# Kernel tuning notes

Measured on AMD Instinct MI355X. Metric: run time of the kernel, lower is better.

The kernel has to match this reference:

```python
import jax, jax.numpy as jnp
import numpy as np

N, H, HEADS = 4096, 256, 3
ALPHA = 0.2
NEG_INF = -9e15


def _sign_adj(key, n, density):
    # sparse signed adjacency with +1 on the diagonal (values in {-1,0,1})
    k1, k2 = jax.random.split(key)
    mask = jax.random.uniform(k1, (n, n)) < density
    sign = jnp.where(jax.random.uniform(k2, (n, n)) < 0.5, -1.0, 1.0)
    adj = jnp.where(mask, sign, 0.0).astype(jnp.float32)
    idx = jnp.arange(n)
    return adj.at[idx, idx].set(1.0)


def setup_inputs() -> dict:
    key = jax.random.key(0)
    ks = jax.random.split(key, 16)
    std = 0.01
    gain = 1.414
    return {
        "h": jax.random.normal(ks[0], (N, H), jnp.float32),
        "node_adj": _sign_adj(ks[1], N, 0.005),
        "edge_adj": _sign_adj(ks[2], N, 0.005),
        "gat_W": jax.random.normal(ks[3], (HEADS, H, H), jnp.float32) * (gain / np.sqrt(H, dtype=np.float32)),
        "gat_a": jax.random.normal(ks[4], (HEADS, 2 * H, 1), jnp.float32) * 0.1,
        "edge_Wih": jax.random.normal(ks[5], (3 * H, H), jnp.float32) * std,
        "edge_Whh": jax.random.normal(ks[6], (3 * H, H), jnp.float32) * std,
        "edge_bih": jnp.zeros((3 * H,), jnp.float32),
        "edge_bhh": jnp.zeros((3 * H,), jnp.float32),
        "node_Wih": jax.random.normal(ks[7], (3 * H, H), jnp.float32) * std,
        "node_Whh": jax.random.normal(ks[8], (3 * H, H), jnp.float32) * std,
        "node_bih": jnp.zeros((3 * H,), jnp.float32),
        "node_bhh": jnp.zeros((3 * H,), jnp.float32),
    }


def _gru_cell(x, hstate, Wih, Whh, bih, bhh):
    # torch.nn.GRUCell math, gate order [r, z, n]
    gi = x @ Wih.T + bih
    gh = hstate @ Whh.T + bhh
    ir, iz, inn = jnp.split(gi, 3, axis=1)
    hr, hz, hn = jnp.split(gh, 3, axis=1)
    r = jax.nn.sigmoid(ir + hr)
    z = jax.nn.sigmoid(iz + hz)
    n = jnp.tanh(inn + r * hn)
    return (1.0 - z) * n + z * hstate


def _gat_head(h, node_adj, edge_adj, W, a):
    hW = h @ W  # [N,H]
    hp = (node_adj > 0).astype(hW.dtype) @ hW
    hm = (node_adj < 0).astype(hW.dtype) @ hW
    e_plus = jax.nn.leaky_relu(jnp.concatenate([hp, hm], axis=1) @ a, ALPHA)[:, 0]   # [N]
    e_minus = jax.nn.leaky_relu(jnp.concatenate([hm, hp], axis=1) @ a, ALPHA)[:, 0]  # [N]
    # attention[i, j] depends only on column j (original builds this via repeat)
    att = jnp.where(edge_adj > 0, e_plus[None, :], NEG_INF)
    att = jnp.where(edge_adj < 0, e_minus[None, :], att)
    att = jax.nn.softmax(att, axis=1)
    return (att * edge_adj) @ hW  # concat=False -> no elu


def reference(h, node_adj, edge_adj, gat_W, gat_a,
              edge_Wih, edge_Whh, edge_bih, edge_bhh,
              node_Wih, node_Whh, node_bih, node_bhh):
    dn = jnp.diag(node_adj)  # [N]
    de = jnp.diag(edge_adj)  # [N]
    idx = jnp.arange(node_adj.shape[0])
    node_adj_norm = node_adj.at[idx, idx].add(-dn)  # zero diagonal
    edge_adj_norm = edge_adj.at[idx, idx].add(-de)

    # msg_type == 'diff'
    node_support = node_adj_norm @ h
    edge_output = _gru_cell(node_support, h, edge_Wih, edge_Whh, edge_bih, edge_bhh)

    edge_support = _gat_head(h, node_adj_norm, edge_adj_norm, gat_W[0], gat_a[0])
    for i in range(1, HEADS):
        edge_support = edge_support + _gat_head(h, node_adj_norm, edge_adj_norm, gat_W[i], gat_a[i])
    edge_support = edge_support / HEADS

    node_output = _gru_cell(edge_support, h, node_Wih, node_Whh, node_bih, node_bhh)

    # sp.mm(I_edge, edge_output) + sp.mm(I_node, node_output)
    return de[:, None] * edge_output + dn[:, None] * node_output
```

## Files before the change

### kernel.cpp

```cpp
#include <hip/hip_runtime.h>
#include <hip/hip_bf16.h>
#include <math.h>

#define NN 4096
#define HH 256
#define G3 768
#define NHEADS 3
#define MAXE 128
#define ALPHA 0.2f

typedef __bf16 bf16;
typedef __attribute__((ext_vector_type(2))) __bf16 bf16x2;
typedef __attribute__((ext_vector_type(4))) __bf16 bf16x4;
typedef __attribute__((ext_vector_type(8))) __bf16 bf16x8;
typedef __attribute__((ext_vector_type(4))) float f32x4;

__device__ __forceinline__ void async_copy16(void* lds, const void* g) {
    __builtin_amdgcn_global_load_lds((const __attribute__((address_space(1))) void*)g,
                                     (__attribute__((address_space(3))) void*)lds, 16, 0, 0);
}

__device__ inline float lrelu(float x) { return x > 0.f ? x : ALPHA * x; }
__device__ inline float sigm(float x) { return 1.f / (1.f + __expf(-x)); }

__global__ __launch_bounds__(256) void prep_k(
    const float* __restrict__ h,
    const float* __restrict__ eWih, const float* __restrict__ eWhh,
    const float* __restrict__ nWih, const float* __restrict__ nWhh,
    const float* __restrict__ gat_W, const float* __restrict__ gat_a,
    bf16* __restrict__ hb,
    bf16* __restrict__ Weib, bf16* __restrict__ Wehb,
    bf16* __restrict__ Wnib, bf16* __restrict__ Wnhb,
    bf16* __restrict__ Wtb, float* __restrict__ c0, float* __restrict__ c1) {
    __shared__ float tile[32][33];
    __shared__ float a_s[512];
    int b = blockIdx.x, t = threadIdx.x;
    if (b < 1024) {
        int idx = b * 256 + t;
        float4 v = *(const float4*)(h + (size_t)idx * 4);
        bf16x4 o = {(bf16)v.x, (bf16)v.y, (bf16)v.z, (bf16)v.w};
        *(bf16x4*)(hb + (size_t)idx * 4) = o;
    } else if (b < 1792) {
        int w = (b - 1024) / 192;
        int idx = ((b - 1024) % 192) * 256 + t;
        const float* in = w == 0 ? eWih : (w == 1 ? eWhh : (w == 2 ? nWih : nWhh));
        bf16* outp = w == 0 ? Weib : (w == 1 ? Wehb : (w == 2 ? Wnib : Wnhb));
        float4 v = *(const float4*)(in + (size_t)idx * 4);
        bf16x4 o = {(bf16)v.x, (bf16)v.y, (bf16)v.z, (bf16)v.w};
        *(bf16x4*)(outp + (size_t)idx * 4) = o;
    } else if (b < 1984) {
        int b2 = b - 1792;
        int hd = b2 >> 6, tl = b2 & 63;
        int k0 = (tl >> 3) * 32, n0 = (tl & 7) * 32;
        int tx = t % 32, ty = t / 32;
        const float* Wh = gat_W + (size_t)hd * HH * HH;
        for (int r = ty; r < 32; r += 8) tile[r][tx] = Wh[(size_t)(k0 + r) * HH + n0 + tx];
        __syncthreads();
        bf16* Wth = Wtb + (size_t)hd * HH * HH;
        for (int r = ty; r < 32; r += 8) Wth[(size_t)(n0 + r) * HH + k0 + tx] = (bf16)tile[tx][r];
    } else {
        int hd = b - 1984;
        a_s[t] = gat_a[(size_t)hd * 512 + t];
        a_s[t + 256] = gat_a[(size_t)hd * 512 + 256 + t];
        __syncthreads();
        const float* Wr = gat_W + (size_t)hd * HH * HH + (size_t)t * HH;
        f32x4 s0v = {}, s1v = {};
#pragma unroll 8
        for (int c4 = 0; c4 < 64; c4++) {
            f32x4 w = *(const f32x4*)(Wr + c4 * 4);
            f32x4 a0 = *(const f32x4*)(a_s + c4 * 4);
            f32x4 a1 = *(const f32x4*)(a_s + 256 + c4 * 4);
            s0v += w * a0;
            s1v += w * a1;
        }
        c0[hd * HH + t] = s0v[0] + s0v[1] + s0v[2] + s0v[3];
        c1[hd * HH + t] = s1v[0] + s1v[1] + s1v[2] + s1v[3];
    }
}

__global__ __launch_bounds__(256) void scan_k(
    const float* __restrict__ node_adj, const float* __restrict__ edge_adj,
    const bf16* __restrict__ hb,
    const float* __restrict__ c0, const float* __restrict__ c1,
    bf16* __restrict__ nsupb, float* __restrict__ dn, float* __restrict__ de,
    float* __restrict__ ep, float* __restrict__ em,
    int* __restrict__ csr_cols, int* __restrict__ csr_nnz) {
    __shared__ float buf[2][NN];
    __shared__ int cnt[2];
    __shared__ int colsbuf[2][MAXE];
    __shared__ float part[6][4];
    int t = threadIdx.x, lane = t & 63, wid = t >> 6;
    int r0 = blockIdx.x * 2;

    if (t == 0) { cnt[0] = 0; cnt[1] = 0; }

    {
        const float* src = node_adj + (size_t)r0 * NN + t * 4;
        float* dst = &buf[0][t * 4];
#pragma unroll
        for (int q = 0; q < 4; q++) async_copy16(dst + q * 1024, src + q * 1024);
    }
    __syncthreads();

#pragma unroll
    for (int tk = 0; tk < 4; tk++) {
        int par = tk & 1;
        int i = r0 + (tk >> 1);
        bool node_t = (par == 0);

        if (tk < 3) {
            int ntk = tk + 1;
            int nrow = r0 + (ntk >> 1);
            const float* src = ((ntk & 1) ? edge_adj : node_adj) + (size_t)nrow * NN + t * 4;
            float* dst = &buf[ntk & 1][t * 4];
#pragma unroll
            for (int q = 0; q < 4; q++) async_copy16(dst + q * 1024, src + q * 1024);
        }

        float wv[16];
#pragma unroll
        for (int q = 0; q < 16; q++) wv[q] = buf[par][q * 256 + t];

        int k = 0;
#pragma unroll
        for (int q = 0; q < 16; q++) {
            int j = q * 256 + t;
            if (wv[q] != 0.f) {
                if (j == i) (node_t ? dn : de)[i] = wv[q];
                else k++;
            }
        }
        int base = 0;
        if (k) base = atomicAdd(&cnt[par], k);
#pragma unroll
        for (int q = 0; q < 16; q++) {
            int j = q * 256 + t;
            if (wv[q] != 0.f && j != i) {
                if (base < MAXE) colsbuf[par][base] = (wv[q] > 0.f) ? (j + 1) : -(j + 1);
                base++;
            }
        }
        __syncthreads();
        int n = cnt[par];
        if (n > MAXE) n = MAXE;

        if (node_t) {
            float accp = 0.f, accm = 0.f;
#pragma unroll 8
            for (int kk = 0; kk < n; kk++) {
                int c = colsbuf[par][kk];
                int j = (c > 0 ? c : -c) - 1;
                float hv = (float)hb[(size_t)j * HH + t];
                if (c > 0) accp += hv; else accm += hv;
            }
            nsupb[(size_t)i * HH + t] = (bf16)(accp - accm);
            float u[6];
#pragma unroll
            for (int hd = 0; hd < NHEADS; hd++) {
                float a0 = c0[hd * HH + t], a1 = c1[hd * HH + t];
                u[hd * 2]     = accp * a0 + accm * a1;
                u[hd * 2 + 1] = accm * a0 + accp * a1;
            }
#pragma unroll
            for (int vv = 0; vv < 6; vv++)
#pragma unroll
                for (int off = 32; off; off >>= 1) u[vv] += __shfl_xor(u[vv], off);
            if (lane == 0)
#pragma unroll
                for (int vv = 0; vv < 6; vv++) part[vv][wid] = u[vv];
            __syncthreads();
            if (t < 6) {
                float s = part[t][0] + part[t][1] + part[t][2] + part[t][3];
                int hd = t >> 1;
                ((t & 1) == 0 ? ep : em)[(size_t)hd * NN + i] = lrelu(s);
            }
        } else {
            if (t == 0) csr_nnz[i] = n;
            if (t < n) csr_cols[(size_t)i * MAXE + t] = colsbuf[par][t];
        }
        __syncthreads();
        if (t == 0) cnt[par] = 0;
    }
}

__global__ __launch_bounds__(256) void gemm_bt(
    const bf16* __restrict__ A0, const bf16* __restrict__ A1, const bf16* __restrict__ A2,
    const bf16* __restrict__ B0, const bf16* __restrict__ B1, const bf16* __restrict__ B2,
    bf16* __restrict__ C0, bf16* __restrict__ C1, bf16* __restrict__ C2) {
    __shared__ bf16 a_s[128 * 32];
    __shared__ bf16 b_s[128 * 32];
    int z = blockIdx.z;
    const bf16* A = z == 0 ? A0 : (z == 1 ? A1 : A2);
    const bf16* Bt = z == 0 ? B0 : (z == 1 ? B1 : B2);
    bf16* C = z == 0 ? C0 : (z == 1 ? C1 : C2);

    int tid = threadIdx.x;
    int lane = tid & 63, wid = tid >> 6;
    int wr = (wid >> 1) * 64, wc = (wid & 1) * 64;
    int i0 = blockIdx.x * 128;
    int c0n = blockIdx.y * 128;

    f32x4 acc[4][4] = {};
    int kq = (lane >> 4) * 8;

    for (int k0 = 0; k0 < 256; k0 += 32) {
        __syncthreads();
#pragma unroll
        for (int it = 0; it < 2; it++) {
            int ch = it * 256 + tid;
            int r = ch >> 2, c16 = ch & 3;
            async_copy16(&a_s[ch * 8], A + (size_t)(i0 + r) * 256 + k0 + c16 * 8);
            async_copy16(&b_s[ch * 8], Bt + (size_t)(c0n + r) * 256 + k0 + c16 * 8);
        }
        __syncthreads();
        bf16x8 af[4], bf[4];
#pragma unroll
        for (int m = 0; m < 4; m++) af[m] = *(const bf16x8*)&a_s[(wr + m * 16 + (lane & 15)) * 32 + kq];
#pragma unroll
        for (int n = 0; n < 4; n++) bf[n] = *(const bf16x8*)&b_s[(wc + n * 16 + (lane & 15)) * 32 + kq];
#pragma unroll
        for (int m = 0; m < 4; m++)
#pragma unroll
            for (int n = 0; n < 4; n++)
                acc[m][n] = __builtin_amdgcn_mfma_f32_16x16x32_bf16(af[m], bf[n], acc[m][n], 0, 0, 0);
    }
#pragma unroll
    for (int m = 0; m < 4; m++) {
#pragma unroll
        for (int n = 0; n < 4; n++) {
            int row = i0 + wr + m * 16 + (lane >> 4) * 4;
            int col = c0n + wc + n * 16 + (lane & 15);
#pragma unroll
            for (int j = 0; j < 4; j++)
                C[(size_t)(row + j) * G3 + col] = (bf16)acc[m][n][j];
        }
    }
}

__global__ __launch_bounds__(256) void gat_out(
    const int* __restrict__ csr_cols, const int* __restrict__ csr_nnz,
    const float* __restrict__ ep, const float* __restrict__ em,
    const bf16* __restrict__ hWb2, bf16* __restrict__ esupb) {
    int i = blockIdx.x, t = threadIdx.x;
    __shared__ int cols_s[MAXE];
    __shared__ int js[MAXE];
    __shared__ float w_s[NHEADS][MAXE];
    __shared__ f32x4 sacc[NHEADS][64];
    int n = csr_nnz[i];
    if (t < n) {
        int c = csr_cols[(size_t)i * MAXE + t];
        cols_s[t] = c;
        js[t] = (c > 0 ? c : -c) - 1;
    }
    __syncthreads();
    int wid = t >> 6, lane = t & 63;
    if (wid < NHEADS) {
        int hd = wid;
        const float* eph = ep + (size_t)hd * NN;
        const float* emh = em + (size_t)hd * NN;
        float v0 = -1e30f, v1 = -1e30f;
        if (lane < n)      { int c = cols_s[lane];      v0 = c > 0 ? eph[js[lane]]      : emh[js[lane]]; }
        if (lane + 64 < n) { int c = cols_s[lane + 64]; v1 = c > 0 ? eph[js[lane + 64]] : emh[js[lane + 64]]; }
        float mx = fmaxf(v0, v1);
#pragma unroll
        for (int off = 32; off; off >>= 1) mx = fmaxf(mx, __shfl_xor(mx, off));
        float w0 = (lane < n) ? __expf(v0 - mx) : 0.f;
        float w1 = (lane + 64 < n) ? __expf(v1 - mx) : 0.f;
        float s = w0 + w1;
#pragma unroll
        for (int off = 32; off; off >>= 1) s += __shfl_xor(s, off);
        float inv = 1.f / s;
        if (lane < n)      w_s[hd][lane]      = (cols_s[lane] > 0 ? w0 : -w0) * inv;
        if (lane + 64 < n) w_s[hd][lane + 64] = (cols_s[lane + 64] > 0 ? w1 : -w1) * inv;
    }
    __syncthreads();
    if (t < 192) {
        int hd = t >> 6, g = t & 63;
        const bf16* base = hWb2 + (size_t)hd * HH + g * 4;
        f32x4 acc = {};
#pragma unroll 4
        for (int k = 0; k < n; k++) {
            float w = w_s[hd][k];
            bf16x4 hv = *(const bf16x4*)(base + (size_t)js[k] * G3);
            f32x4 f = {(float)hv[0], (float)hv[1], (float)hv[2], (float)hv[3]};
            acc += w * f;
        }
        sacc[hd][g] = acc;
    }
    __syncthreads();
    if (t < 64) {
        f32x4 s = (sacc[0][t] + sacc[1][t] + sacc[2][t]) * (1.f / 3.f);
        bf16x4 o = {(bf16)s[0], (bf16)s[1], (bf16)s[2], (bf16)s[3]};
        *(bf16x4*)(esupb + (size_t)i * HH + t * 4) = o;
    }
}

__global__ __launch_bounds__(256) void gru_both(
    const bf16* __restrict__ gie, const bf16* __restrict__ ghe,
    const bf16* __restrict__ gin, const bf16* __restrict__ ghn,
    const float* __restrict__ ebih, const float* __restrict__ ebhh,
    const float* __restrict__ nbih, const float* __restrict__ nbhh,
    const float* __restrict__ h, const float* __restrict__ dnv, const float* __restrict__ dev,
    float* __restrict__ out) {
    int sub = threadIdx.x >> 7, tc = threadIdx.x & 127;
    int i = blockIdx.x * 2 + sub;
    int c = tc * 2;
    size_t gb = (size_t)i * G3;
    float2 hv = *(const float2*)(h + (size_t)i * HH + c);
    float De = dev[i], Dn = dnv[i];

#define LD2(p, off) (*(const bf16x2*)((p) + gb + (off) + c))
#define BI2(p, off) (*(const float2*)((p) + (off) + c))
    bf16x2 eir = LD2(gie, 0), eiz = LD2(gie, 256), ein = LD2(gie, 512);
    bf16x2 ehr = LD2(ghe, 0), ehz = LD2(ghe, 256), ehn = LD2(ghe, 512);
    bf16x2 nir = LD2(gin, 0), niz = LD2(gin, 256), nin = LD2(gin, 512);
    bf16x2 nhr = LD2(ghn, 0), nhz = LD2(ghn, 256), nhn = LD2(ghn, 512);
    float2 ebr = BI2(ebih, 0), ebz = BI2(ebih, 256), ebn = BI2(ebih, 512);
    float2 eb2r = BI2(ebhh, 0), eb2z = BI2(ebhh, 256), eb2n = BI2(ebhh, 512);
    float2 nbr = BI2(nbih, 0), nbz = BI2(nbih, 256), nbn = BI2(nbih, 512);
    float2 nb2r = BI2(nbhh, 0), nb2z = BI2(nbhh, 256), nb2n = BI2(nbhh, 512);
#undef LD2
#undef BI2

    float res[2];
#pragma unroll
    for (int j = 0; j < 2; j++) {
        float hj = j == 0 ? hv.x : hv.y;
        float r = sigm(((float)eir[j] + (j ? ebr.y : ebr.x)) + ((float)ehr[j] + (j ? eb2r.y : eb2r.x)));
        float z = sigm(((float)eiz[j] + (j ? ebz.y : ebz.x)) + ((float)ehz[j] + (j ? eb2z.y : eb2z.x)));
        float nv = tanhf(((float)ein[j] + (j ? ebn.y : ebn.x)) + r * ((float)ehn[j] + (j ? eb2n.y : eb2n.x)));
        float eo = (1.f - z) * nv + z * hj;
        float r2 = sigm(((float)nir[j] + (j ? nbr.y : nbr.x)) + ((float)nhr[j] + (j ? nb2r.y : nb2r.x)));
        float z2 = sigm(((float)niz[j] + (j ? nbz.y : nbz.x)) + ((float)nhz[j] + (j ? nb2z.y : nb2z.x)));
        float nv2 = tanhf(((float)nin[j] + (j ? nbn.y : nbn.x)) + r2 * ((float)nhn[j] + (j ? nb2n.y : nb2n.x)));
        float no = (1.f - z2) * nv2 + z2 * hj;
        res[j] = De * eo + Dn * no;
    }
    *(float2*)(out + (size_t)i * HH + c) = make_float2(res[0], res[1]);
}

extern "C" void kernel_launch(void* const* d_in, const int* in_sizes, int n_in,
                              void* d_out, int out_size, void* d_ws, size_t ws_size,
                              hipStream_t stream) {
    const float* h        = (const float*)d_in[0];
    const float* node_adj = (const float*)d_in[1];
    const float* edge_adj = (const float*)d_in[2];
    const float* gat_W    = (const float*)d_in[3];
    const float* gat_a    = (const float*)d_in[4];
    const float* e_Wih    = (const float*)d_in[5];
    const float* e_Whh    = (const float*)d_in[6];
    const float* e_bih    = (const float*)d_in[7];
    const float* e_bhh    = (const float*)d_in[8];
    const float* n_Wih    = (const float*)d_in[9];
    const float* n_Whh    = (const float*)d_in[10];
    const float* n_bih    = (const float*)d_in[11];
    const float* n_bhh    = (const float*)d_in[12];
    float* out = (float*)d_out;

    char* ws = (char*)d_ws;
    size_t off = 0;
    auto alloc = [&](size_t bytes) { char* p = ws + off; off += (bytes + 255) & ~(size_t)255; return p; };

    float* ep    = (float*)alloc((size_t)NHEADS * NN * 4);
    float* em    = (float*)alloc((size_t)NHEADS * NN * 4);
    float* c0    = (float*)alloc((size_t)NHEADS * HH * 4);
    float* c1    = (float*)alloc((size_t)NHEADS * HH * 4);
    float* dn    = (float*)alloc(NN * 4);
    float* de    = (float*)alloc(NN * 4);
    bf16*  hb    = (bf16*)alloc((size_t)NN * HH * 2);
    bf16*  nsupb = (bf16*)alloc((size_t)NN * HH * 2);
    bf16*  esupb = (bf16*)alloc((size_t)NN * HH * 2);
    bf16*  hWb2  = (bf16*)alloc((size_t)NN * G3 * 2);
    bf16*  gie   = (bf16*)alloc((size_t)NN * G3 * 2);
    bf16*  ghe   = (bf16*)alloc((size_t)NN * G3 * 2);
    bf16*  gin   = (bf16*)alloc((size_t)NN * G3 * 2);
    bf16*  ghn   = (bf16*)alloc((size_t)NN * G3 * 2);
    bf16*  Weib  = (bf16*)alloc((size_t)G3 * HH * 2);
    bf16*  Wehb  = (bf16*)alloc((size_t)G3 * HH * 2);
    bf16*  Wnib  = (bf16*)alloc((size_t)G3 * HH * 2);
    bf16*  Wnhb  = (bf16*)alloc((size_t)G3 * HH * 2);
    bf16*  Wtb   = (bf16*)alloc((size_t)NHEADS * HH * HH * 2);
    int*   csr_cols = (int*)alloc((size_t)NN * MAXE * 4);
    int*   csr_nnz  = (int*)alloc(NN * 4);

    dim3 b256(256);

    prep_k<<<1987, b256, 0, stream>>>(h, e_Wih, e_Whh, n_Wih, n_Whh, gat_W, gat_a,
                                      hb, Weib, Wehb, Wnib, Wnhb, Wtb, c0, c1);

    scan_k<<<NN / 2, b256, 0, stream>>>(node_adj, edge_adj, hb, c0, c1,
                                        nsupb, dn, de, ep, em, csr_cols, csr_nnz);

    gemm_bt<<<dim3(NN / 128, G3 / 128, 3), b256, 0, stream>>>(
        hb, nsupb, hb, Wtb, Weib, Wehb, hWb2, gie, ghe);

    gat_out<<<NN, b256, 0, stream>>>(csr_cols, csr_nnz, ep, em, hWb2, esupb);

    gemm_bt<<<dim3(NN / 128, G3 / 128, 2), b256, 0, stream>>>(
        esupb, hb, hb, Wnib, Wnhb, Wnhb, gin, ghn, ghn);

    gru_both<<<NN / 2, b256, 0, stream>>>(gie, ghe, gin, ghn,
                                          e_bih, e_bhh, n_bih, n_bhh,
                                          h, dn, de, out);
}
```

Baseline: 101.2 us.

## Split adjacency scan into standalone compaction kernel and separate gather kernel

Replaces the fused scan kernel, which double-buffered node and edge adjacency rows through LDS and then gathered neighbour features, with two kernels. A compaction kernel with one block per row (8192 blocks) reads each row with direct vector loads and writes signed column lists, and a separate gather kernel accumulates the h neighbour sums and attention logits. The goal is more parallelism and memory-level concurrency for the 128 MB adjacency stream, and independence from the prep kernel. The cost is an extra launch and an extra round trip of the column lists through global memory. The column order inside each row now depends on per-thread chunking rather than strided ownership, which can change the summation order.

```diff
diff --git a/kernel.cpp b/kernel.cpp
--- a/kernel.cpp
+++ b/kernel.cpp
@@ -78,108 +78,92 @@
     }
 }
 
-__global__ __launch_bounds__(256) void scan_k(
+__global__ __launch_bounds__(256) void compact_k(
     const float* __restrict__ node_adj, const float* __restrict__ edge_adj,
+    float* __restrict__ dn, float* __restrict__ de,
+    int* __restrict__ ccols_n, int* __restrict__ nnz_n,
+    int* __restrict__ ccols_e, int* __restrict__ nnz_e) {
+    int b = blockIdx.x, t = threadIdx.x;
+    bool node = b < NN;
+    int i = node ? b : b - NN;
+    __shared__ int cnt;
+    __shared__ int cols_s[MAXE];
+    if (t == 0) cnt = 0;
+    __syncthreads();
+    const float* rp = (node ? node_adj : edge_adj) + (size_t)i * NN + t * 16;
+
+    f32x4 v0 = *(const f32x4*)(rp);
+    f32x4 v1 = *(const f32x4*)(rp + 4);
+    f32x4 v2 = *(const f32x4*)(rp + 8);
+    f32x4 v3 = *(const f32x4*)(rp + 12);
+    int j0 = t * 16;
+
+    int k = 0;
+#define CNT(A, J) { float a_ = (A); if (a_ != 0.f) { if ((J) == i) (node ? dn : de)[i] = a_; else k++; } }
+    CNT(v0[0], j0)      CNT(v0[1], j0 + 1)  CNT(v0[2], j0 + 2)  CNT(v0[3], j0 + 3)
+    CNT(v1[0], j0 + 4)  CNT(v1[1], j0 + 5)  CNT(v1[2], j0 + 6)  CNT(v1[3], j0 + 7)
+    CNT(v2[0], j0 + 8)  CNT(v2[1], j0 + 9)  CNT(v2[2], j0 + 10) CNT(v2[3], j0 + 11)
+    CNT(v3[0], j0 + 12) CNT(v3[1], j0 + 13) CNT(v3[2], j0 + 14) CNT(v3[3], j0 + 15)
+#undef CNT
+
+    int base = 0;
+    if (k) base = atomicAdd(&cnt, k);
+
+#define WRT(A, J) { float a_ = (A); if (a_ != 0.f && (J) != i) { \
+        if (base < MAXE) cols_s[base] = (a_ > 0.f) ? ((J) + 1) : -((J) + 1); base++; } }
+    WRT(v0[0], j0)      WRT(v0[1], j0 + 1)  WRT(v0[2], j0 + 2)  WRT(v0[3], j0 + 3)
+    WRT(v1[0], j0 + 4)  WRT(v1[1], j0 + 5)  WRT(v1[2], j0 + 6)  WRT(v1[3], j0 + 7)
+    WRT(v2[0], j0 + 8)  WRT(v2[1], j0 + 9)  WRT(v2[2], j0 + 10) WRT(v2[3], j0 + 11)
+    WRT(v3[0], j0 + 12) WRT(v3[1], j0 + 13) WRT(v3[2], j0 + 14) WRT(v3[3], j0 + 15)
+#undef WRT
+
+    __syncthreads();
+    int n = cnt < MAXE ? cnt : MAXE;
+    int* cg = (node ? ccols_n : ccols_e) + (size_t)i * MAXE;
+    if (t == 0) (node ? nnz_n : nnz_e)[i] = n;
+    if (t < n) cg[t] = cols_s[t];
+}
+
+__global__ __launch_bounds__(256) void gather_k(
+    const int* __restrict__ ccols_n, const int* __restrict__ nnz_n,
     const bf16* __restrict__ hb,
     const float* __restrict__ c0, const float* __restrict__ c1,
-    bf16* __restrict__ nsupb, float* __restrict__ dn, float* __restrict__ de,
-    float* __restrict__ ep, float* __restrict__ em,
-    int* __restrict__ csr_cols, int* __restrict__ csr_nnz) {
-    __shared__ float buf[2][NN];
-    __shared__ int cnt[2];
-    __shared__ int colsbuf[2][MAXE];
+    bf16* __restrict__ nsupb, float* __restrict__ ep, float* __restrict__ em) {
+    int i = blockIdx.x, t = threadIdx.x, lane = t & 63, wid = t >> 6;
+    __shared__ int cols_s[MAXE];
     __shared__ float part[6][4];
-    int t = threadIdx.x, lane = t & 63, wid = t >> 6;
-    int r0 = blockIdx.x * 2;
-
-    if (t == 0) { cnt[0] = 0; cnt[1] = 0; }
-
-    {
-        const float* src = node_adj + (size_t)r0 * NN + t * 4;
-        float* dst = &buf[0][t * 4];
-#pragma unroll
-        for (int q = 0; q < 4; q++) async_copy16(dst + q * 1024, src + q * 1024);
-    }
-    __syncthreads();
-
-#pragma unroll
-    for (int tk = 0; tk < 4; tk++) {
-        int par = tk & 1;
-        int i = r0 + (tk >> 1);
-        bool node_t = (par == 0);
-
-        if (tk < 3) {
-            int ntk = tk + 1;
-            int nrow = r0 + (ntk >> 1);
-            const float* src = ((ntk & 1) ? edge_adj : node_adj) + (size_t)nrow * NN + t * 4;
-            float* dst = &buf[ntk & 1][t * 4];
-#pragma unroll
-            for (int q = 0; q < 4; q++) async_copy16(dst + q * 1024, src + q * 1024);
-        }
-
-        float wv[16];
-#pragma unroll
-        for (int q = 0; q < 16; q++) wv[q] = buf[par][q * 256 + t];
-
-        int k = 0;
-#pragma unroll
-        for (int q = 0; q < 16; q++) {
-            int j = q * 256 + t;
-            if (wv[q] != 0.f) {
-                if (j == i) (node_t ? dn : de)[i] = wv[q];
-                else k++;
-            }
-        }
-        int base = 0;
-        if (k) base = atomicAdd(&cnt[par], k);
-#pragma unroll
-        for (int q = 0; q < 16; q++) {
-            int j = q * 256 + t;
-            if (wv[q] != 0.f && j != i) {
-                if (base < MAXE) colsbuf[par][base] = (wv[q] > 0.f) ? (j + 1) : -(j + 1);
-                base++;
-            }
-        }
-        __syncthreads();
-        int n = cnt[par];
-        if (n > MAXE) n = MAXE;
-
-        if (node_t) {
-            float accp = 0.f, accm = 0.f;
+    int n = nnz_n[i];
+    if (n > MAXE) n = MAXE;
+    if (t < n) cols_s[t] = ccols_n[(size_t)i * MAXE + t];
+    __syncthreads();
+    float accp = 0.f, accm = 0.f;
 #pragma unroll 8
-            for (int kk = 0; kk < n; kk++) {
-                int c = colsbuf[par][kk];
-                int j = (c > 0 ? c : -c) - 1;
-                float hv = (float)hb[(size_t)j * HH + t];
-                if (c > 0) accp += hv; else accm += hv;
-            }
-            nsupb[(size_t)i * HH + t] = (bf16)(accp - accm);
-            float u[6];
-#pragma unroll
-            for (int hd = 0; hd < NHEADS; hd++) {
-                float a0 = c0[hd * HH + t], a1 = c1[hd * HH + t];
-                u[hd * 2]     = accp * a0 + accm * a1;
-                u[hd * 2 + 1] = accm * a0 + accp * a1;
-            }
-#pragma unroll
-            for (int vv = 0; vv < 6; vv++)
-#pragma unroll
-                for (int off = 32; off; off >>= 1) u[vv] += __shfl_xor(u[vv], off);
-            if (lane == 0)
-#pragma unroll
-                for (int vv = 0; vv < 6; vv++) part[vv][wid] = u[vv];
-            __syncthreads();
-            if (t < 6) {
-                float s = part[t][0] + part[t][1] + part[t][2] + part[t][3];
-                int hd = t >> 1;
-                ((t & 1) == 0 ? ep : em)[(size_t)hd * NN + i] = lrelu(s);
-            }
-        } else {
-            if (t == 0) csr_nnz[i] = n;
-            if (t < n) csr_cols[(size_t)i * MAXE + t] = colsbuf[par][t];
-        }
-        __syncthreads();
-        if (t == 0) cnt[par] = 0;
+    for (int kk = 0; kk < n; kk++) {
+        int c = cols_s[kk];
+        int j = (c > 0 ? c : -c) - 1;
+        float hv = (float)hb[(size_t)j * HH + t];
+        if (c > 0) accp += hv; else accm += hv;
+    }
+    nsupb[(size_t)i * HH + t] = (bf16)(accp - accm);
+    float u[6];
+#pragma unroll
+    for (int hd = 0; hd < NHEADS; hd++) {
+        float a0 = c0[hd * HH + t], a1 = c1[hd * HH + t];
+        u[hd * 2]     = accp * a0 + accm * a1;
+        u[hd * 2 + 1] = accm * a0 + accp * a1;
+    }
+#pragma unroll
+    for (int vv = 0; vv < 6; vv++)
+#pragma unroll
+        for (int off = 32; off; off >>= 1) u[vv] += __shfl_xor(u[vv], off);
+    if (lane == 0)
+#pragma unroll
+        for (int vv = 0; vv < 6; vv++) part[vv][wid] = u[vv];
+    __syncthreads();
+    if (t < 6) {
+        float s = part[t][0] + part[t][1] + part[t][2] + part[t][3];
+        int hd = t >> 1;
+        ((t & 1) == 0 ? ep : em)[(size_t)hd * NN + i] = lrelu(s);
     }
 }
 
@@ -238,7 +222,7 @@
 }
 
 __global__ __launch_bounds__(256) void gat_out(
-    const int* __restrict__ csr_cols, const int* __restrict__ csr_nnz,
+    const int* __restrict__ ccols_e, const int* __restrict__ nnz_e,
     const float* __restrict__ ep, const float* __restrict__ em,
     const bf16* __restrict__ hWb2, bf16* __restrict__ esupb) {
     int i = blockIdx.x, t = threadIdx.x;
@@ -246,9 +230,10 @@
     __shared__ int js[MAXE];
     __shared__ float w_s[NHEADS][MAXE];
     __shared__ f32x4 sacc[NHEADS][64];
-    int n = csr_nnz[i];
+    int n = nnz_e[i];
+    if (n > MAXE) n = MAXE;
     if (t < n) {
-        int c = csr_cols[(size_t)i * MAXE + t];
+        int c = ccols_e[(size_t)i * MAXE + t];
         cols_s[t] = c;
         js[t] = (c > 0 ? c : -c) - 1;
     }
@@ -380,21 +365,25 @@
     bf16*  Wnib  = (bf16*)alloc((size_t)G3 * HH * 2);
     bf16*  Wnhb  = (bf16*)alloc((size_t)G3 * HH * 2);
     bf16*  Wtb   = (bf16*)alloc((size_t)NHEADS * HH * HH * 2);
-    int*   csr_cols = (int*)alloc((size_t)NN * MAXE * 4);
-    int*   csr_nnz  = (int*)alloc(NN * 4);
+    int*   ccols_n = (int*)alloc((size_t)NN * MAXE * 4);
+    int*   nnz_n   = (int*)alloc(NN * 4);
+    int*   ccols_e = (int*)alloc((size_t)NN * MAXE * 4);
+    int*   nnz_e   = (int*)alloc(NN * 4);
 
     dim3 b256(256);
+
+    compact_k<<<2 * NN, b256, 0, stream>>>(node_adj, edge_adj, dn, de,
+                                           ccols_n, nnz_n, ccols_e, nnz_e);
 
     prep_k<<<1987, b256, 0, stream>>>(h, e_Wih, e_Whh, n_Wih, n_Whh, gat_W, gat_a,
                                       hb, Weib, Wehb, Wnib, Wnhb, Wtb, c0, c1);
 
-    scan_k<<<NN / 2, b256, 0, stream>>>(node_adj, edge_adj, hb, c0, c1,
-                                        nsupb, dn, de, ep, em, csr_cols, csr_nnz);
+    gather_k<<<NN, b256, 0, stream>>>(ccols_n, nnz_n, hb, c0, c1, nsupb, ep, em);
 
     gemm_bt<<<dim3(NN / 128, G3 / 128, 3), b256, 0, stream>>>(
         hb, nsupb, hb, Wtb, Weib, Wehb, hWb2, gie, ghe);
 
-    gat_out<<<NN, b256, 0, stream>>>(csr_cols, csr_nnz, ep, em, hWb2, esupb);
+    gat_out<<<NN, b256, 0, stream>>>(ccols_e, nnz_e, ep, em, hWb2, esupb);
 
     gemm_bt<<<dim3(NN / 128, G3 / 128, 2), b256, 0, stream>>>(
         esupb, hb, hb, Wnib, Wnhb, Wnhb, gin, ghn, ghn);
```

New measurement: 95.43 us. 5.7% less time.
